# Kernel tuning notes

Measured on AMD Instinct MI355X. Metric: run time of the kernel, lower is better.

## Reference

```python
import jax, jax.numpy as jnp
import numpy as np

B, S, H, L = 64, 512, 768, 32  # batch, seq_len, bert hidden, clauses per doc


def setup_inputs() -> dict:
    key = jax.random.key(0)
    k1, k2, k3, k4 = jax.random.split(key, 4)
    sequence_output = jax.random.normal(k1, (B, S, H), jnp.float32)
    context_h = jax.random.normal(k2, (B, H), jnp.float32)
    # clause boundary positions (SEP indices); pos[0]=0, evenly spaced clauses
    step = (S - 2) // L  # 15 tokens per clause, pos[L]=480 < S-1
    clauses_positions = jnp.tile(jnp.arange(L + 1, dtype=jnp.int32) * step, (B, 1))
    doc_lens = jnp.full((B,), L, dtype=jnp.int32)
    D = 2 * H  # 1536: [clause_mean ; CLS]
    W_pool = jax.random.normal(k3, (D, D), jnp.float32) / np.sqrt(D).astype(np.float32)
    b_pool = jnp.zeros((D,), jnp.float32)
    W_out = jax.random.normal(k4, (D,), jnp.float32) / np.sqrt(D).astype(np.float32)
    b_out = jnp.zeros((), jnp.float32)
    return dict(sequence_output=sequence_output, context_h=context_h,
                W_pool=W_pool, b_pool=b_pool, W_out=W_out, b_out=b_out,
                clauses_positions=clauses_positions, doc_lens=doc_lens)


def reference(sequence_output, context_h, W_pool, b_pool, W_out, b_out,
              clauses_positions, doc_lens):
    # clause i (1..L) covers tokens [pos[i-1]+1, pos[i]]; last clause also
    # includes pos[L]+1 (split_size[-1] += 1 in the torch code).
    starts = clauses_positions[:, :-1] + 1           # [B, L]
    ends = clauses_positions[:, 1:] + 1              # exclusive
    ends = ends.at[:, -1].add(1)                     # last clause gets the SEP
    t = jnp.arange(sequence_output.shape[1])         # [S]
    seg_mask = ((t[None, None, :] >= starts[:, :, None]) &
                (t[None, None, :] < ends[:, :, None]))          # [B, L, S]
    counts = (ends - starts).astype(sequence_output.dtype)      # [B, L]
    sums = jnp.einsum('bls,bsh->blh', seg_mask.astype(sequence_output.dtype),
                      sequence_output)                          # segment sums
    means = sums / counts[:, :, None]                           # [B, L, H]
    cls = jnp.broadcast_to(sequence_output[:, :1, :], means.shape)
    clause_h = jnp.concatenate([means, cls], axis=-1)           # [B, L, 2H]
    pooled = jnp.tanh(clause_h @ W_pool.T + b_pool)             # Pooler
    logits = pooled @ W_out + b_out                             # [B, L]
    return logits
```

## Files before the change

kernel.cpp:

```cpp
#include <hip/hip_runtime.h>
#include <hip/hip_bf16.h>

#define SS 512
#define HH 768
#define LL 32
#define DD 1536
#define MM 2048
#define KK DD

typedef float f32x4 __attribute__((ext_vector_type(4)));
typedef short bf16x8 __attribute__((ext_vector_type(8)));

__device__ __forceinline__ unsigned short f2bf(float x) {
    union { float f; unsigned u; } v; v.f = x;
    unsigned r = v.u + 0x7fff + ((v.u >> 16) & 1);
    return (unsigned short)(r >> 16);
}

__device__ __forceinline__ void gload16(const unsigned short* g, unsigned short* l) {
    __builtin_amdgcn_global_load_lds(
        (const __attribute__((address_space(1))) void*)g,
        (__attribute__((address_space(3))) void*)l, 16, 0, 0);
}

__global__ __launch_bounds__(192)
void prep(const float* __restrict__ seq, const int* __restrict__ pos,
          const float* __restrict__ Wp, const float* __restrict__ bo,
          unsigned short* __restrict__ Abf, unsigned short* __restrict__ Wbf,
          float* __restrict__ out) {
    const int blk = blockIdx.x;
    const int tid = threadIdx.x;
    if (blk < MM) {
        int b = blk >> 5;
        int l = blk & 31;
        const int* pb = pos + b * (LL + 1);
        int start = pb[l] + 1;
        int end   = pb[l + 1] + 1;
        if (l == LL - 1) end += 1;
        float inv = 1.0f / (float)(end - start);
        const float* base = seq + (size_t)b * SS * HH;
        float4 a = make_float4(0.f, 0.f, 0.f, 0.f);
        for (int t = start; t < end; ++t) {
            float4 v = reinterpret_cast<const float4*>(base + (size_t)t * HH)[tid];
            a.x += v.x; a.y += v.y; a.z += v.z; a.w += v.w;
        }
        unsigned short* o = Abf + (size_t)blk * DD;
        ushort4 m;
        m.x = f2bf(a.x * inv); m.y = f2bf(a.y * inv);
        m.z = f2bf(a.z * inv); m.w = f2bf(a.w * inv);
        reinterpret_cast<ushort4*>(o)[tid] = m;
        float4 c = reinterpret_cast<const float4*>(base)[tid];
        ushort4 cc;
        cc.x = f2bf(c.x); cc.y = f2bf(c.y); cc.z = f2bf(c.z); cc.w = f2bf(c.w);
        reinterpret_cast<ushort4*>(o + HH)[tid] = cc;
    } else if (blk < MM + 3072) {
        int i = ((blk - MM) * 192 + tid) * 4;
        float4 v = *(const float4*)(Wp + i);
        ushort4 o;
        o.x = f2bf(v.x); o.y = f2bf(v.y); o.z = f2bf(v.z); o.w = f2bf(v.w);
        *(ushort4*)(Wbf + i) = o;
    } else {
        int i = (blk - MM - 3072) * 192 + tid;
        if (i < MM) out[i] = bo[0];
    }
}

__global__ __launch_bounds__(256, 3)
void gemm_mfma(const unsigned short* __restrict__ A,
               const unsigned short* __restrict__ Bm,
               const float* __restrict__ bp,
               const float* __restrict__ Wo,
               float* __restrict__ out) {
    __shared__ unsigned short As[3 * 4096];
    __shared__ unsigned short Bs[3 * 4096];
    const int tid  = threadIdx.x;
    const int wid  = tid >> 6;
    const int lane = tid & 63;
    const int fr   = lane & 15;
    const int fq   = lane >> 4;
    const int wr   = wid >> 1, wc = wid & 1;

    const int blk = blockIdx.x;
    const int c = blk & 7;
    const int i = blk >> 3;
    const int bm = ((c >> 1) << 3) + (i & 7);
    const int bn = (c & 1) * 12 + (i >> 3);
    const int brow = bm * 64;
    const int bcol = bn * 64;

    const int srow = tid >> 3;
    const int sc   = (tid & 7) ^ (srow & 7);
    const unsigned short* gA = A  + (size_t)(brow + srow) * KK + sc * 8;
    const unsigned short* gB = Bm + (size_t)(bcol + srow) * KK + sc * 8;
    unsigned short* asW = As + wid * 512;
    unsigned short* bsW = Bs + wid * 512;

#define STAGE(buf, kt) do {                                          \
        gload16(gA + (kt) * 64,           asW + (buf) * 4096);       \
        gload16(gA + (kt) * 64 + 32 * KK, asW + (buf) * 4096 + 2048);\
        gload16(gB + (kt) * 64,           bsW + (buf) * 4096);       \
        gload16(gB + (kt) * 64 + 32 * KK, bsW + (buf) * 4096 + 2048);\
    } while (0)

    const int s0 = fq ^ (fr & 7);
    const int s1 = s0 ^ 4;
    const int rA = wr * 32 + fr;
    const int rB = wc * 32 + fr;
    const int oA00 = rA * 64 + s0 * 8, oA01 = rA * 64 + s1 * 8;
    const int oA10 = oA00 + 16 * 64,   oA11 = oA01 + 16 * 64;
    const int oB00 = rB * 64 + s0 * 8, oB01 = rB * 64 + s1 * 8;
    const int oB10 = oB00 + 16 * 64,   oB11 = oB01 + 16 * 64;

    f32x4 acc[2][2] = {};

    STAGE(0, 0); STAGE(1, 1);

#define BODY(t, buf) do {                                                     \
        __builtin_amdgcn_sched_barrier(0);                                    \
        if ((t) <= 22) asm volatile("s_waitcnt vmcnt(4)" ::: "memory");       \
        else           asm volatile("s_waitcnt vmcnt(0)" ::: "memory");       \
        __builtin_amdgcn_s_barrier();                                         \
        __builtin_amdgcn_sched_barrier(0);                                    \
        if ((t) + 2 < 24) STAGE(((t) + 2) % 3, (t) + 2);                      \
        const unsigned short* as_ = As + (buf) * 4096;                        \
        const unsigned short* bs_ = Bs + (buf) * 4096;                        \
        bf16x8 a00 = *(const bf16x8*)(as_ + oA00);                            \
        bf16x8 a01 = *(const bf16x8*)(as_ + oA01);                            \
        bf16x8 a10 = *(const bf16x8*)(as_ + oA10);                            \
        bf16x8 a11 = *(const bf16x8*)(as_ + oA11);                            \
        bf16x8 b00 = *(const bf16x8*)(bs_ + oB00);                            \
        bf16x8 b01 = *(const bf16x8*)(bs_ + oB01);                            \
        bf16x8 b10 = *(const bf16x8*)(bs_ + oB10);                            \
        bf16x8 b11 = *(const bf16x8*)(bs_ + oB11);                            \
        __builtin_amdgcn_s_setprio(1);                                        \
        acc[0][0] = __builtin_amdgcn_mfma_f32_16x16x32_bf16(a00, b00, acc[0][0], 0, 0, 0); \
        acc[0][0] = __builtin_amdgcn_mfma_f32_16x16x32_bf16(a01, b01, acc[0][0], 0, 0, 0); \
        acc[0][1] = __builtin_amdgcn_mfma_f32_16x16x32_bf16(a00, b10, acc[0][1], 0, 0, 0); \
        acc[0][1] = __builtin_amdgcn_mfma_f32_16x16x32_bf16(a01, b11, acc[0][1], 0, 0, 0); \
        acc[1][0] = __builtin_amdgcn_mfma_f32_16x16x32_bf16(a10, b00, acc[1][0], 0, 0, 0); \
        acc[1][0] = __builtin_amdgcn_mfma_f32_16x16x32_bf16(a11, b01, acc[1][0], 0, 0, 0); \
        acc[1][1] = __builtin_amdgcn_mfma_f32_16x16x32_bf16(a10, b10, acc[1][1], 0, 0, 0); \
        acc[1][1] = __builtin_amdgcn_mfma_f32_16x16x32_bf16(a11, b11, acc[1][1], 0, 0, 0); \
        __builtin_amdgcn_s_setprio(0);                                        \
    } while (0)

    #pragma unroll
    for (int t = 0; t < 24; ++t) {
        BODY(t, t % 3);
    }
#undef BODY
#undef STAGE

    #pragma unroll
    for (int m = 0; m < 2; ++m) {
        float vsum[4] = {0.f, 0.f, 0.f, 0.f};
        #pragma unroll
        for (int n = 0; n < 2; ++n) {
            const int col = bcol + wc * 32 + n * 16 + fr;
            const float wo_ = Wo[col];
            const float pb_ = bp[col];
            #pragma unroll
            for (int r = 0; r < 4; ++r) {
                float x = acc[m][n][r] + pb_;
                float th = 1.f - 2.f / (__expf(2.f * x) + 1.f);
                vsum[r] += th * wo_;
            }
        }
        #pragma unroll
        for (int r = 0; r < 4; ++r) {
            float v = vsum[r];
            v += __shfl_xor(v, 1, 16);
            v += __shfl_xor(v, 2, 16);
            v += __shfl_xor(v, 4, 16);
            v += __shfl_xor(v, 8, 16);
            if (fr == 0)
                atomicAdd(&out[brow + wr * 32 + m * 16 + fq * 4 + r], v);
        }
    }
}

extern "C" void kernel_launch(void* const* d_in, const int* in_sizes, int n_in,
                              void* d_out, int out_size, void* d_ws, size_t ws_size,
                              hipStream_t stream) {
    const float* seq   = (const float*)d_in[0];
    const float* Wp    = (const float*)d_in[2];
    const float* bp    = (const float*)d_in[3];
    const float* Wo    = (const float*)d_in[4];
    const float* bo    = (const float*)d_in[5];
    const int*   pos   = (const int*)d_in[6];
    float* out = (float*)d_out;

    unsigned short* Abf = (unsigned short*)d_ws;
    unsigned short* Wbf = Abf + (size_t)MM * DD;

    const int ninit = (MM + 191) / 192;
    prep<<<MM + 3072 + ninit, 192, 0, stream>>>(seq, pos, Wp, bo, Abf, Wbf, out);
    gemm_mfma<<<768, 256, 0, stream>>>(Abf, Wbf, bp, Wo, out);
}
```

Before: 42.13 us.

## Enlarge GEMM tiles to 128x96 with double-buffered LDS pipeline

Raises the GEMM block tile from 64x64 to 128x96, with each wave computing a 64x48 sub-tile (4x3 MFMA accumulators). This improves operand reuse from LDS and cuts global/L2 traffic. The pipeline changes from triple buffering with a partial vmcnt wait to double buffering that waits on all loads each step. The grid shrinks from 768 to 256 blocks, which matches the 256 CUs but reduces latency hiding and occupancy. The XCD-aware block mapping is adjusted to the new tile counts.

```diff
diff --git a/kernel.cpp b/kernel.cpp
--- a/kernel.cpp
+++ b/kernel.cpp
@@ -7,6 +7,11 @@
 #define DD 1536
 #define MM 2048
 #define KK DD
+
+#define BM 128
+#define BN 96
+#define BK 64
+#define NSTEP (KK / BK)
 
 typedef float f32x4 __attribute__((ext_vector_type(4)));
 typedef short bf16x8 __attribute__((ext_vector_type(8)));
@@ -65,14 +70,14 @@
     }
 }
 
-__global__ __launch_bounds__(256, 3)
+__global__ __launch_bounds__(256, 2)
 void gemm_mfma(const unsigned short* __restrict__ A,
                const unsigned short* __restrict__ Bm,
                const float* __restrict__ bp,
                const float* __restrict__ Wo,
                float* __restrict__ out) {
-    __shared__ unsigned short As[3 * 4096];
-    __shared__ unsigned short Bs[3 * 4096];
+    __shared__ unsigned short As[2][BM * BK];
+    __shared__ unsigned short Bs[2][BN * BK];
     const int tid  = threadIdx.x;
     const int wid  = tid >> 6;
     const int lane = tid & 63;
@@ -81,82 +86,84 @@
     const int wr   = wid >> 1, wc = wid & 1;
 
     const int blk = blockIdx.x;
-    const int c = blk & 7;
-    const int i = blk >> 3;
-    const int bm = ((c >> 1) << 3) + (i & 7);
-    const int bn = (c & 1) * 12 + (i >> 3);
-    const int brow = bm * 64;
-    const int bcol = bn * 64;
-
-    const int srow = tid >> 3;
-    const int sc   = (tid & 7) ^ (srow & 7);
-    const unsigned short* gA = A  + (size_t)(brow + srow) * KK + sc * 8;
-    const unsigned short* gB = Bm + (size_t)(bcol + srow) * KK + sc * 8;
-    unsigned short* asW = As + wid * 512;
-    unsigned short* bsW = Bs + wid * 512;
-
-#define STAGE(buf, kt) do {                                          \
-        gload16(gA + (kt) * 64,           asW + (buf) * 4096);       \
-        gload16(gA + (kt) * 64 + 32 * KK, asW + (buf) * 4096 + 2048);\
-        gload16(gB + (kt) * 64,           bsW + (buf) * 4096);       \
-        gload16(gB + (kt) * 64 + 32 * KK, bsW + (buf) * 4096 + 2048);\
+    const int xcd = blk & 7;
+    const int ii  = blk >> 3;
+    const int bm  = (xcd >> 1) * 4 + (ii & 3);
+    const int bn  = (xcd & 1) * 8 + (ii >> 2);
+    const int brow = bm * BM;
+    const int bcol = bn * BN;
+
+    const int lr  = lane >> 3;
+    const int sch = (lane & 7) ^ lr;
+    const unsigned short* gA = A  + (size_t)(brow + wid * 32 + lr) * KK + sch * 8;
+    const unsigned short* gB = Bm + (size_t)(bcol + wid * 24 + lr) * KK + sch * 8;
+
+#define STAGE(buf, t) do {                                                    \
+        _Pragma("unroll")                                                     \
+        for (int j = 0; j < 4; ++j)                                           \
+            gload16(gA + (size_t)j * 8 * KK + (t) * 64,                       \
+                    &As[buf][(wid * 32 + j * 8) * 64]);                       \
+        _Pragma("unroll")                                                     \
+        for (int j = 0; j < 3; ++j)                                           \
+            gload16(gB + (size_t)j * 8 * KK + (t) * 64,                       \
+                    &Bs[buf][(wid * 24 + j * 8) * 64]);                       \
     } while (0)
 
     const int s0 = fq ^ (fr & 7);
     const int s1 = s0 ^ 4;
-    const int rA = wr * 32 + fr;
-    const int rB = wc * 32 + fr;
-    const int oA00 = rA * 64 + s0 * 8, oA01 = rA * 64 + s1 * 8;
-    const int oA10 = oA00 + 16 * 64,   oA11 = oA01 + 16 * 64;
-    const int oB00 = rB * 64 + s0 * 8, oB01 = rB * 64 + s1 * 8;
-    const int oB10 = oB00 + 16 * 64,   oB11 = oB01 + 16 * 64;
-
-    f32x4 acc[2][2] = {};
-
-    STAGE(0, 0); STAGE(1, 1);
-
-#define BODY(t, buf) do {                                                     \
-        __builtin_amdgcn_sched_barrier(0);                                    \
-        if ((t) <= 22) asm volatile("s_waitcnt vmcnt(4)" ::: "memory");       \
-        else           asm volatile("s_waitcnt vmcnt(0)" ::: "memory");       \
-        __builtin_amdgcn_s_barrier();                                         \
-        __builtin_amdgcn_sched_barrier(0);                                    \
-        if ((t) + 2 < 24) STAGE(((t) + 2) % 3, (t) + 2);                      \
-        const unsigned short* as_ = As + (buf) * 4096;                        \
-        const unsigned short* bs_ = Bs + (buf) * 4096;                        \
-        bf16x8 a00 = *(const bf16x8*)(as_ + oA00);                            \
-        bf16x8 a01 = *(const bf16x8*)(as_ + oA01);                            \
-        bf16x8 a10 = *(const bf16x8*)(as_ + oA10);                            \
-        bf16x8 a11 = *(const bf16x8*)(as_ + oA11);                            \
-        bf16x8 b00 = *(const bf16x8*)(bs_ + oB00);                            \
-        bf16x8 b01 = *(const bf16x8*)(bs_ + oB01);                            \
-        bf16x8 b10 = *(const bf16x8*)(bs_ + oB10);                            \
-        bf16x8 b11 = *(const bf16x8*)(bs_ + oB11);                            \
-        __builtin_amdgcn_s_setprio(1);                                        \
-        acc[0][0] = __builtin_amdgcn_mfma_f32_16x16x32_bf16(a00, b00, acc[0][0], 0, 0, 0); \
-        acc[0][0] = __builtin_amdgcn_mfma_f32_16x16x32_bf16(a01, b01, acc[0][0], 0, 0, 0); \
-        acc[0][1] = __builtin_amdgcn_mfma_f32_16x16x32_bf16(a00, b10, acc[0][1], 0, 0, 0); \
-        acc[0][1] = __builtin_amdgcn_mfma_f32_16x16x32_bf16(a01, b11, acc[0][1], 0, 0, 0); \
-        acc[1][0] = __builtin_amdgcn_mfma_f32_16x16x32_bf16(a10, b00, acc[1][0], 0, 0, 0); \
-        acc[1][0] = __builtin_amdgcn_mfma_f32_16x16x32_bf16(a11, b01, acc[1][0], 0, 0, 0); \
-        acc[1][1] = __builtin_amdgcn_mfma_f32_16x16x32_bf16(a10, b10, acc[1][1], 0, 0, 0); \
-        acc[1][1] = __builtin_amdgcn_mfma_f32_16x16x32_bf16(a11, b11, acc[1][1], 0, 0, 0); \
-        __builtin_amdgcn_s_setprio(0);                                        \
-    } while (0)
-
-    #pragma unroll
-    for (int t = 0; t < 24; ++t) {
-        BODY(t, t % 3);
-    }
-#undef BODY
+    int oA0[4], oA1[4], oB0[3], oB1[3];
+    #pragma unroll
+    for (int m = 0; m < 4; ++m) {
+        int r = (wr * 64 + m * 16 + fr) * 64;
+        oA0[m] = r + s0 * 8; oA1[m] = r + s1 * 8;
+    }
+    #pragma unroll
+    for (int n = 0; n < 3; ++n) {
+        int r = (wc * 48 + n * 16 + fr) * 64;
+        oB0[n] = r + s0 * 8; oB1[n] = r + s1 * 8;
+    }
+
+    f32x4 acc[4][3] = {};
+
+    STAGE(0, 0);
+
+    #pragma unroll
+    for (int t = 0; t < NSTEP; ++t) {
+        const int buf = t & 1;
+        __builtin_amdgcn_sched_barrier(0);
+        asm volatile("s_waitcnt vmcnt(0)" ::: "memory");
+        __builtin_amdgcn_s_barrier();
+        __builtin_amdgcn_sched_barrier(0);
+        if (t + 1 < NSTEP) STAGE(buf ^ 1, t + 1);
+        const unsigned short* as_ = As[buf];
+        const unsigned short* bs_ = Bs[buf];
+        #pragma unroll
+        for (int h = 0; h < 2; ++h) {
+            bf16x8 a[4], b[3];
+            #pragma unroll
+            for (int m = 0; m < 4; ++m)
+                a[m] = *(const bf16x8*)(as_ + (h ? oA1[m] : oA0[m]));
+            #pragma unroll
+            for (int n = 0; n < 3; ++n)
+                b[n] = *(const bf16x8*)(bs_ + (h ? oB1[n] : oB0[n]));
+            __builtin_amdgcn_s_setprio(1);
+            #pragma unroll
+            for (int m = 0; m < 4; ++m)
+                #pragma unroll
+                for (int n = 0; n < 3; ++n)
+                    acc[m][n] = __builtin_amdgcn_mfma_f32_16x16x32_bf16(
+                        a[m], b[n], acc[m][n], 0, 0, 0);
+            __builtin_amdgcn_s_setprio(0);
+        }
+    }
 #undef STAGE
 
     #pragma unroll
-    for (int m = 0; m < 2; ++m) {
+    for (int m = 0; m < 4; ++m) {
         float vsum[4] = {0.f, 0.f, 0.f, 0.f};
         #pragma unroll
-        for (int n = 0; n < 2; ++n) {
-            const int col = bcol + wc * 32 + n * 16 + fr;
+        for (int n = 0; n < 3; ++n) {
+            const int col = bcol + wc * 48 + n * 16 + fr;
             const float wo_ = Wo[col];
             const float pb_ = bp[col];
             #pragma unroll
@@ -174,7 +181,7 @@
             v += __shfl_xor(v, 4, 16);
             v += __shfl_xor(v, 8, 16);
             if (fr == 0)
-                atomicAdd(&out[brow + wr * 32 + m * 16 + fq * 4 + r], v);
+                atomicAdd(&out[brow + wr * 64 + m * 16 + fq * 4 + r], v);
         }
     }
 }
@@ -195,5 +202,5 @@
 
     const int ninit = (MM + 191) / 192;
     prep<<<MM + 3072 + ninit, 192, 0, stream>>>(seq, pos, Wp, bo, Abf, Wbf, out);
-    gemm_mfma<<<768, 256, 0, stream>>>(Abf, Wbf, bp, Wo, out);
-}
+    gemm_mfma<<<256, 256, 0, stream>>>(Abf, Wbf, bp, Wo, out);
+}
```

Result: slower. 49.66 us (+17.9%).

## Split K across two wave groups per GEMM tile with 128-wide K stages

Applied to the files above, without the earlier changes.

The GEMM block grows from 4 to 8 waves. The two halves of the block each handle half of every 128-element K slice, and their partial accumulators are reduced through LDS before the tanh/dot epilogue. The staging pipeline changes from triple-buffered 64-wide K steps to double-buffered 128-wide steps, with plain __syncthreads in place of hand-tuned vmcnt waits, and the XOR swizzle widens to 16 chunks. This is meant to give more waves per tile to hide latency and halve the number of K iterations, at the cost of an extra LDS reduction, shallower prefetch and higher register/LDS pressure per block.

```diff
diff --git a/kernel.cpp b/kernel.cpp
--- a/kernel.cpp
+++ b/kernel.cpp
@@ -7,6 +7,7 @@
 #define DD 1536
 #define MM 2048
 #define KK DD
+#define NMS 12
 
 typedef float f32x4 __attribute__((ext_vector_type(4)));
 typedef short bf16x8 __attribute__((ext_vector_type(8)));
@@ -65,20 +66,22 @@
     }
 }
 
-__global__ __launch_bounds__(256, 3)
+__global__ __launch_bounds__(512, 4)
 void gemm_mfma(const unsigned short* __restrict__ A,
                const unsigned short* __restrict__ Bm,
                const float* __restrict__ bp,
                const float* __restrict__ Wo,
                float* __restrict__ out) {
-    __shared__ unsigned short As[3 * 4096];
-    __shared__ unsigned short Bs[3 * 4096];
+    __shared__ unsigned short As[2 * 8192];
+    __shared__ unsigned short Bs[2 * 8192];
     const int tid  = threadIdx.x;
     const int wid  = tid >> 6;
     const int lane = tid & 63;
     const int fr   = lane & 15;
     const int fq   = lane >> 4;
-    const int wr   = wid >> 1, wc = wid & 1;
+    const int ks   = wid >> 2;
+    const int w2   = wid & 3;
+    const int wr   = w2 >> 1, wc = w2 & 1;
 
     const int blk = blockIdx.x;
     const int c = blk & 7;
@@ -88,80 +91,82 @@
     const int brow = bm * 64;
     const int bcol = bn * 64;
 
-    const int srow = tid >> 3;
-    const int sc   = (tid & 7) ^ (srow & 7);
-    const unsigned short* gA = A  + (size_t)(brow + srow) * KK + sc * 8;
-    const unsigned short* gB = Bm + (size_t)(bcol + srow) * KK + sc * 8;
-    unsigned short* asW = As + wid * 512;
-    unsigned short* bsW = Bs + wid * 512;
-
-#define STAGE(buf, kt) do {                                          \
-        gload16(gA + (kt) * 64,           asW + (buf) * 4096);       \
-        gload16(gA + (kt) * 64 + 32 * KK, asW + (buf) * 4096 + 2048);\
-        gload16(gB + (kt) * 64,           bsW + (buf) * 4096);       \
-        gload16(gB + (kt) * 64 + 32 * KK, bsW + (buf) * 4096 + 2048);\
+    const int l16 = lane >> 4;
+    const int c16 = lane & 15;
+    const int row0 = wid * 8 + l16;
+    const int row1 = row0 + 4;
+    const unsigned short* gA0 = A  + (size_t)(brow + row0) * KK + (c16 ^ (row0 & 15)) * 8;
+    const unsigned short* gA1 = A  + (size_t)(brow + row1) * KK + (c16 ^ (row1 & 15)) * 8;
+    const unsigned short* gB0 = Bm + (size_t)(bcol + row0) * KK + (c16 ^ (row0 & 15)) * 8;
+    const unsigned short* gB1 = Bm + (size_t)(bcol + row1) * KK + (c16 ^ (row1 & 15)) * 8;
+
+#define STAGE(buf, t) do {                                            \
+        gload16(gA0 + (t) * 128, &As[(buf) * 8192 + wid * 1024]);     \
+        gload16(gA1 + (t) * 128, &As[(buf) * 8192 + wid * 1024 + 512]);\
+        gload16(gB0 + (t) * 128, &Bs[(buf) * 8192 + wid * 1024]);     \
+        gload16(gB1 + (t) * 128, &Bs[(buf) * 8192 + wid * 1024 + 512]);\
     } while (0)
 
-    const int s0 = fq ^ (fr & 7);
-    const int s1 = s0 ^ 4;
-    const int rA = wr * 32 + fr;
-    const int rB = wc * 32 + fr;
-    const int oA00 = rA * 64 + s0 * 8, oA01 = rA * 64 + s1 * 8;
-    const int oA10 = oA00 + 16 * 64,   oA11 = oA01 + 16 * 64;
-    const int oB00 = rB * 64 + s0 * 8, oB01 = rB * 64 + s1 * 8;
-    const int oB10 = oB00 + 16 * 64,   oB11 = oB01 + 16 * 64;
+    const int kb = ks * 8;
+    int oA[2][2], oB[2][2];
+    #pragma unroll
+    for (int m = 0; m < 2; ++m)
+        #pragma unroll
+        for (int h = 0; h < 2; ++h) {
+            oA[m][h] = (wr * 32 + m * 16 + fr) * 128 + ((kb + h * 4 + fq) ^ fr) * 8;
+            oB[m][h] = (wc * 32 + m * 16 + fr) * 128 + ((kb + h * 4 + fq) ^ fr) * 8;
+        }
 
     f32x4 acc[2][2] = {};
 
-    STAGE(0, 0); STAGE(1, 1);
-
-#define BODY(t, buf) do {                                                     \
-        __builtin_amdgcn_sched_barrier(0);                                    \
-        if ((t) <= 22) asm volatile("s_waitcnt vmcnt(4)" ::: "memory");       \
-        else           asm volatile("s_waitcnt vmcnt(0)" ::: "memory");       \
-        __builtin_amdgcn_s_barrier();                                         \
-        __builtin_amdgcn_sched_barrier(0);                                    \
-        if ((t) + 2 < 24) STAGE(((t) + 2) % 3, (t) + 2);                      \
-        const unsigned short* as_ = As + (buf) * 4096;                        \
-        const unsigned short* bs_ = Bs + (buf) * 4096;                        \
-        bf16x8 a00 = *(const bf16x8*)(as_ + oA00);                            \
-        bf16x8 a01 = *(const bf16x8*)(as_ + oA01);                            \
-        bf16x8 a10 = *(const bf16x8*)(as_ + oA10);                            \
-        bf16x8 a11 = *(const bf16x8*)(as_ + oA11);                            \
-        bf16x8 b00 = *(const bf16x8*)(bs_ + oB00);                            \
-        bf16x8 b01 = *(const bf16x8*)(bs_ + oB01);                            \
-        bf16x8 b10 = *(const bf16x8*)(bs_ + oB10);                            \
-        bf16x8 b11 = *(const bf16x8*)(bs_ + oB11);                            \
-        __builtin_amdgcn_s_setprio(1);                                        \
-        acc[0][0] = __builtin_amdgcn_mfma_f32_16x16x32_bf16(a00, b00, acc[0][0], 0, 0, 0); \
-        acc[0][0] = __builtin_amdgcn_mfma_f32_16x16x32_bf16(a01, b01, acc[0][0], 0, 0, 0); \
-        acc[0][1] = __builtin_amdgcn_mfma_f32_16x16x32_bf16(a00, b10, acc[0][1], 0, 0, 0); \
-        acc[0][1] = __builtin_amdgcn_mfma_f32_16x16x32_bf16(a01, b11, acc[0][1], 0, 0, 0); \
-        acc[1][0] = __builtin_amdgcn_mfma_f32_16x16x32_bf16(a10, b00, acc[1][0], 0, 0, 0); \
-        acc[1][0] = __builtin_amdgcn_mfma_f32_16x16x32_bf16(a11, b01, acc[1][0], 0, 0, 0); \
-        acc[1][1] = __builtin_amdgcn_mfma_f32_16x16x32_bf16(a10, b10, acc[1][1], 0, 0, 0); \
-        acc[1][1] = __builtin_amdgcn_mfma_f32_16x16x32_bf16(a11, b11, acc[1][1], 0, 0, 0); \
-        __builtin_amdgcn_s_setprio(0);                                        \
-    } while (0)
+    STAGE(0, 0);
 
     #pragma unroll
-    for (int t = 0; t < 24; ++t) {
-        BODY(t, t % 3);
-    }
-#undef BODY
+    for (int t = 0; t < NMS; ++t) {
+        const int buf = t & 1;
+        __syncthreads();
+        if (t + 1 < NMS) STAGE(buf ^ 1, t + 1);
+        const unsigned short* as_ = As + buf * 8192;
+        const unsigned short* bs_ = Bs + buf * 8192;
+        #pragma unroll
+        for (int h = 0; h < 2; ++h) {
+            bf16x8 a0 = *(const bf16x8*)(as_ + oA[0][h]);
+            bf16x8 a1 = *(const bf16x8*)(as_ + oA[1][h]);
+            bf16x8 b0 = *(const bf16x8*)(bs_ + oB[0][h]);
+            bf16x8 b1 = *(const bf16x8*)(bs_ + oB[1][h]);
+            acc[0][0] = __builtin_amdgcn_mfma_f32_16x16x32_bf16(a0, b0, acc[0][0], 0, 0, 0);
+            acc[0][1] = __builtin_amdgcn_mfma_f32_16x16x32_bf16(a0, b1, acc[0][1], 0, 0, 0);
+            acc[1][0] = __builtin_amdgcn_mfma_f32_16x16x32_bf16(a1, b0, acc[1][0], 0, 0, 0);
+            acc[1][1] = __builtin_amdgcn_mfma_f32_16x16x32_bf16(a1, b1, acc[1][1], 0, 0, 0);
+        }
+    }
 #undef STAGE
+
+    __syncthreads();
+    float* xch = (float*)As;
+    if (ks == 1) {
+        #pragma unroll
+        for (int m = 0; m < 2; ++m)
+            #pragma unroll
+            for (int n = 0; n < 2; ++n)
+                *(f32x4*)&xch[(((w2 * 4 + m * 2 + n) * 64) + lane) * 4] = acc[m][n];
+    }
+    __syncthreads();
+    if (ks == 1) return;
 
     #pragma unroll
     for (int m = 0; m < 2; ++m) {
         float vsum[4] = {0.f, 0.f, 0.f, 0.f};
         #pragma unroll
         for (int n = 0; n < 2; ++n) {
+            f32x4 s = acc[m][n] +
+                *(const f32x4*)&xch[(((w2 * 4 + m * 2 + n) * 64) + lane) * 4];
             const int col = bcol + wc * 32 + n * 16 + fr;
             const float wo_ = Wo[col];
             const float pb_ = bp[col];
             #pragma unroll
             for (int r = 0; r < 4; ++r) {
-                float x = acc[m][n][r] + pb_;
+                float x = s[r] + pb_;
                 float th = 1.f - 2.f / (__expf(2.f * x) + 1.f);
                 vsum[r] += th * wo_;
             }
@@ -195,5 +200,5 @@
 
     const int ninit = (MM + 191) / 192;
     prep<<<MM + 3072 + ninit, 192, 0, stream>>>(seq, pos, Wp, bo, Abf, Wbf, out);
-    gemm_mfma<<<768, 256, 0, stream>>>(Abf, Wbf, bp, Wo, out);
-}
+    gemm_mfma<<<768, 512, 0, stream>>>(Abf, Wbf, bp, Wo, out);
+}
```

Measured after the change: 51.65 us. 1.23x slower.

## Split CLS half of pooler GEMM into per-batch dot products

Applied to the files above, without the earlier changes.

Every clause row in a batch shares the same CLS vector, so the CLS half of the pooler matmul is identical across those rows. The GEMM K dimension is halved to 768 (only clause means), and each block separately computes the CLS contribution for its two batches and 64 columns with scalar bf16 dot products added into the epilogue bias. This removes half of the MFMA work and the duplicated CLS rows in the A buffer. In exchange, each block now runs a 384-element scalar FMA prologue plus an extra barrier before its pipeline starts.

```diff
diff --git a/kernel.cpp b/kernel.cpp
--- a/kernel.cpp
+++ b/kernel.cpp
@@ -6,7 +6,8 @@
 #define LL 32
 #define DD 1536
 #define MM 2048
-#define KK DD
+#define KA 768
+#define NSTEP 12
 
 typedef float f32x4 __attribute__((ext_vector_type(4)));
 typedef short bf16x8 __attribute__((ext_vector_type(8)));
@@ -17,6 +18,10 @@
     return (unsigned short)(r >> 16);
 }
 
+__device__ __forceinline__ float bf2f(unsigned short x) {
+    union { unsigned u; float f; } t; t.u = ((unsigned)x) << 16; return t.f;
+}
+
 __device__ __forceinline__ void gload16(const unsigned short* g, unsigned short* l) {
     __builtin_amdgcn_global_load_lds(
         (const __attribute__((address_space(1))) void*)g,
@@ -27,7 +32,7 @@
 void prep(const float* __restrict__ seq, const int* __restrict__ pos,
           const float* __restrict__ Wp, const float* __restrict__ bo,
           unsigned short* __restrict__ Abf, unsigned short* __restrict__ Wbf,
-          float* __restrict__ out) {
+          unsigned short* __restrict__ Cls, float* __restrict__ out) {
     const int blk = blockIdx.x;
     const int tid = threadIdx.x;
     if (blk < MM) {
@@ -44,23 +49,24 @@
             float4 v = reinterpret_cast<const float4*>(base + (size_t)t * HH)[tid];
             a.x += v.x; a.y += v.y; a.z += v.z; a.w += v.w;
         }
-        unsigned short* o = Abf + (size_t)blk * DD;
         ushort4 m;
         m.x = f2bf(a.x * inv); m.y = f2bf(a.y * inv);
         m.z = f2bf(a.z * inv); m.w = f2bf(a.w * inv);
-        reinterpret_cast<ushort4*>(o)[tid] = m;
-        float4 c = reinterpret_cast<const float4*>(base)[tid];
-        ushort4 cc;
-        cc.x = f2bf(c.x); cc.y = f2bf(c.y); cc.z = f2bf(c.z); cc.w = f2bf(c.w);
-        reinterpret_cast<ushort4*>(o + HH)[tid] = cc;
+        reinterpret_cast<ushort4*>(Abf + (size_t)blk * KA)[tid] = m;
     } else if (blk < MM + 3072) {
         int i = ((blk - MM) * 192 + tid) * 4;
         float4 v = *(const float4*)(Wp + i);
         ushort4 o;
         o.x = f2bf(v.x); o.y = f2bf(v.y); o.z = f2bf(v.z); o.w = f2bf(v.w);
         *(ushort4*)(Wbf + i) = o;
+    } else if (blk < MM + 3072 + 64) {
+        int b = blk - MM - 3072;
+        float4 c = reinterpret_cast<const float4*>(seq + (size_t)b * SS * HH)[tid];
+        ushort4 cc;
+        cc.x = f2bf(c.x); cc.y = f2bf(c.y); cc.z = f2bf(c.z); cc.w = f2bf(c.w);
+        reinterpret_cast<ushort4*>(Cls + (size_t)b * KA)[tid] = cc;
     } else {
-        int i = (blk - MM - 3072) * 192 + tid;
+        int i = (blk - MM - 3072 - 64) * 192 + tid;
         if (i < MM) out[i] = bo[0];
     }
 }
@@ -68,11 +74,14 @@
 __global__ __launch_bounds__(256, 3)
 void gemm_mfma(const unsigned short* __restrict__ A,
                const unsigned short* __restrict__ Bm,
+               const unsigned short* __restrict__ Cl,
                const float* __restrict__ bp,
                const float* __restrict__ Wo,
                float* __restrict__ out) {
     __shared__ unsigned short As[3 * 4096];
     __shared__ unsigned short Bs[3 * 4096];
+    __shared__ float c2p[256];
+    __shared__ float c2s[2][64];
     const int tid  = threadIdx.x;
     const int wid  = tid >> 6;
     const int lane = tid & 63;
@@ -88,18 +97,40 @@
     const int brow = bm * 64;
     const int bcol = bn * 64;
 
+    {
+        const int v = tid & 127;
+        const int cb = v >> 6;
+        const int cn = v & 63;
+        const int h  = tid >> 7;
+        const unsigned short* crow = Cl + (size_t)(2 * bm + cb) * KA + h * 384;
+        const unsigned short* wrow = Bm + (size_t)(bcol + cn) * DD + 768 + h * 384;
+        float s = 0.f;
+        #pragma unroll 4
+        for (int kc = 0; kc < 48; ++kc) {
+            bf16x8 av = *(const bf16x8*)(crow + kc * 8);
+            bf16x8 bv = *(const bf16x8*)(wrow + kc * 8);
+            #pragma unroll
+            for (int e = 0; e < 8; ++e)
+                s = fmaf(bf2f((unsigned short)av[e]),
+                         bf2f((unsigned short)bv[e]), s);
+        }
+        c2p[tid] = s;
+    }
+    __syncthreads();
+    if (tid < 128) c2s[tid >> 6][tid & 63] = c2p[tid] + c2p[tid + 128];
+
     const int srow = tid >> 3;
     const int sc   = (tid & 7) ^ (srow & 7);
-    const unsigned short* gA = A  + (size_t)(brow + srow) * KK + sc * 8;
-    const unsigned short* gB = Bm + (size_t)(bcol + srow) * KK + sc * 8;
+    const unsigned short* gA = A  + (size_t)(brow + srow) * KA + sc * 8;
+    const unsigned short* gB = Bm + (size_t)(bcol + srow) * DD + sc * 8;
     unsigned short* asW = As + wid * 512;
     unsigned short* bsW = Bs + wid * 512;
 
 #define STAGE(buf, kt) do {                                          \
         gload16(gA + (kt) * 64,           asW + (buf) * 4096);       \
-        gload16(gA + (kt) * 64 + 32 * KK, asW + (buf) * 4096 + 2048);\
+        gload16(gA + (kt) * 64 + 32 * KA, asW + (buf) * 4096 + 2048);\
         gload16(gB + (kt) * 64,           bsW + (buf) * 4096);       \
-        gload16(gB + (kt) * 64 + 32 * KK, bsW + (buf) * 4096 + 2048);\
+        gload16(gB + (kt) * 64 + 32 * DD, bsW + (buf) * 4096 + 2048);\
     } while (0)
 
     const int s0 = fq ^ (fr & 7);
@@ -113,15 +144,16 @@
 
     f32x4 acc[2][2] = {};
 
+    __syncthreads();
     STAGE(0, 0); STAGE(1, 1);
 
 #define BODY(t, buf) do {                                                     \
         __builtin_amdgcn_sched_barrier(0);                                    \
-        if ((t) <= 22) asm volatile("s_waitcnt vmcnt(4)" ::: "memory");       \
-        else           asm volatile("s_waitcnt vmcnt(0)" ::: "memory");       \
+        if ((t) < NSTEP - 1) asm volatile("s_waitcnt vmcnt(4)" ::: "memory"); \
+        else                 asm volatile("s_waitcnt vmcnt(0)" ::: "memory"); \
         __builtin_amdgcn_s_barrier();                                         \
         __builtin_amdgcn_sched_barrier(0);                                    \
-        if ((t) + 2 < 24) STAGE(((t) + 2) % 3, (t) + 2);                      \
+        if ((t) + 2 < NSTEP) STAGE(((t) + 2) % 3, (t) + 2);                   \
         const unsigned short* as_ = As + (buf) * 4096;                        \
         const unsigned short* bs_ = Bs + (buf) * 4096;                        \
         bf16x8 a00 = *(const bf16x8*)(as_ + oA00);                            \
@@ -145,7 +177,7 @@
     } while (0)
 
     #pragma unroll
-    for (int t = 0; t < 24; ++t) {
+    for (int t = 0; t < NSTEP; ++t) {
         BODY(t, t % 3);
     }
 #undef BODY
@@ -156,12 +188,13 @@
         float vsum[4] = {0.f, 0.f, 0.f, 0.f};
         #pragma unroll
         for (int n = 0; n < 2; ++n) {
-            const int col = bcol + wc * 32 + n * 16 + fr;
+            const int lc  = wc * 32 + n * 16 + fr;
+            const int col = bcol + lc;
             const float wo_ = Wo[col];
-            const float pb_ = bp[col];
+            const float ad_ = bp[col] + c2s[wr][lc];
             #pragma unroll
             for (int r = 0; r < 4; ++r) {
-                float x = acc[m][n][r] + pb_;
+                float x = acc[m][n][r] + ad_;
                 float th = 1.f - 2.f / (__expf(2.f * x) + 1.f);
                 vsum[r] += th * wo_;
             }
@@ -191,9 +224,11 @@
     float* out = (float*)d_out;
 
     unsigned short* Abf = (unsigned short*)d_ws;
-    unsigned short* Wbf = Abf + (size_t)MM * DD;
+    unsigned short* Wbf = Abf + (size_t)MM * KA;
+    unsigned short* Cls = Wbf + (size_t)DD * DD;
 
     const int ninit = (MM + 191) / 192;
-    prep<<<MM + 3072 + ninit, 192, 0, stream>>>(seq, pos, Wp, bo, Abf, Wbf, out);
-    gemm_mfma<<<768, 256, 0, stream>>>(Abf, Wbf, bp, Wo, out);
-}
+    prep<<<MM + 3072 + 64 + ninit, 192, 0, stream>>>(seq, pos, Wp, bo,
+                                                     Abf, Wbf, Cls, out);
+    gemm_mfma<<<768, 256, 0, stream>>>(Abf, Wbf, Cls, bp, Wo, out);
+}
```

After: 54.94 us. 1.3x slower.
